# Kernel tuning notes

Measured on AMD Instinct MI355X. Metric: run time of the kernel, lower is better.

Reference implementation:

```python
import jax, jax.numpy as jnp
import numpy as np
from jax import lax

STEPLIM = 10
TOL = 1e-4
EPS = 1e-12


def setup_inputs() -> dict:
    key = jax.random.key(0)
    k1, k2 = jax.random.split(key)
    psrc = jax.random.normal(k1, (8, 2048, 3), dtype=jnp.float32)
    ptgt = jax.random.normal(k2, (8, 2048, 3), dtype=jnp.float32)
    return {"psrc": psrc, "ptgt": ptgt}


def _kabsch(p, q):
    # Rigid transform (R, t) minimizing ||q - (R p + t)|| via SVD (Kabsch).
    # p, q: [B, N, 3] matched point pairs.
    cs = jnp.mean(p, axis=-2, keepdims=True)  # [B,1,3]
    ct = jnp.mean(q, axis=-2, keepdims=True)
    H = jnp.einsum('bni,bnj->bij', p - cs, q - ct)  # [B,3,3]
    U, S, Vt = jnp.linalg.svd(H, full_matrices=False)
    V = jnp.swapaxes(Vt, -1, -2)
    Ut = jnp.swapaxes(U, -1, -2)
    d = jnp.sign(jnp.linalg.det(V @ Ut))  # [B], reflection fix
    scale = jnp.stack([jnp.ones_like(d), jnp.ones_like(d), d], axis=-1)  # [B,3]
    R = (V * scale[:, None, :]) @ Ut  # V @ diag(1,1,d) @ U^T
    t = ct[:, 0, :] - jnp.einsum('bij,bj->bi', R, cs[:, 0, :])
    return R, t


def _nn(pc, ptgt):
    # Brute-force 1-NN of each pc point in ptgt. Returns (dist [B,Ns], idx [B,Ns]).
    # GEMM-form squared distances: ||a||^2 + ||b||^2 - 2 a.b
    a2 = jnp.sum(pc * pc, axis=-1)  # [B,Ns]
    b2 = jnp.sum(ptgt * ptgt, axis=-1)  # [B,Nt]
    d2 = a2[:, :, None] + b2[:, None, :] - 2.0 * jnp.einsum('bnd,bmd->bnm', pc, ptgt)
    d2 = jnp.maximum(d2, EPS)
    idx = jnp.argmin(d2, axis=-1)  # [B,Ns]
    dist = jnp.sqrt(jnp.min(d2, axis=-1))
    return dist, idx


def reference(psrc, ptgt):
    B = psrc.shape[0]

    def step(carry, _):
        pc, err, done = carry
        dist, idx = _nn(pc, ptgt)
        errnew = jnp.mean(dist, axis=-1)  # [B]
        done_new = jnp.logical_or(done, jnp.all(jnp.abs(errnew - err) < TOL))
        matched = jnp.take_along_axis(ptgt, idx[:, :, None], axis=1)  # [B,Ns,3]
        R, t = _kabsch(pc, matched)
        pc_upd = jnp.einsum('bij,bnj->bni', R, pc) + t[:, None, :]
        pc_new = jnp.where(done_new, pc, pc_upd)
        err_new = jnp.where(done_new, err, errnew)
        return (pc_new, err_new, done_new), None

    init = (psrc, jnp.zeros((B,), psrc.dtype), jnp.array(False))
    (pc_final, _, _), _ = lax.scan(step, init, None, length=STEPLIM)

    # Final transform from original psrc to converged point cloud.
    R, t = _kabsch(psrc, pc_final)
    return jnp.concatenate([R, t[:, :, None]], axis=-1)  # [B,3,4]
```

## Files before the change

### kernel.cpp

```cpp
#include <hip/hip_runtime.h>
#include <math.h>

#define NB 8
#define NP 2048
#define GRID 256
#define THREADS 512
#define TOLF 1e-4f
#define EPSF 1e-12f

#define AL(p)   __hip_atomic_load((p), __ATOMIC_RELAXED, __HIP_MEMORY_SCOPE_AGENT)
#define AS(p,v) __hip_atomic_store((p), (v), __ATOMIC_RELAXED, __HIP_MEMORY_SCOPE_AGENT)

__device__ inline float3 xform_pt(const float* __restrict__ T,
                                  float x, float y, float z) {
    float3 r;
    r.x = fmaf(T[0], x, fmaf(T[1], y, fmaf(T[2], z, T[9])));
    r.y = fmaf(T[3], x, fmaf(T[4], y, fmaf(T[5], z, T[10])));
    r.z = fmaf(T[6], x, fmaf(T[7], y, fmaf(T[8], z, T[11])));
    return r;
}

__device__ void kabsch3x3(const double Spq[9], const double Sp[3], const double Sq[3],
                          double R[9], double t[3]) {
    const double invN = 1.0 / (double)NP;
    double cs[3], ct[3];
#pragma unroll
    for (int i = 0; i < 3; ++i) { cs[i] = Sp[i] * invN; ct[i] = Sq[i] * invN; }
    double Hd[9];
#pragma unroll
    for (int i = 0; i < 3; ++i)
#pragma unroll
        for (int j = 0; j < 3; ++j)
            Hd[i * 3 + j] = Spq[i * 3 + j] - (double)NP * cs[i] * ct[j];

    float Bc[3][3], V[3][3];
#pragma unroll
    for (int j = 0; j < 3; ++j)
#pragma unroll
        for (int i = 0; i < 3; ++i) {
            Bc[j][i] = (float)Hd[i * 3 + j];
            V[j][i]  = (i == j) ? 1.0f : 0.0f;
        }
    for (int sweep = 0; sweep < 12; ++sweep) {
        bool rotated = false;
        for (int p = 0; p < 2; ++p)
            for (int q = p + 1; q < 3; ++q) {
                float app = 0.f, aqq = 0.f, apq = 0.f;
#pragma unroll
                for (int i = 0; i < 3; ++i) {
                    app = fmaf(Bc[p][i], Bc[p][i], app);
                    aqq = fmaf(Bc[q][i], Bc[q][i], aqq);
                    apq = fmaf(Bc[p][i], Bc[q][i], apq);
                }
                if (apq * apq > 1e-24f + 1e-12f * app * aqq) {
                    rotated = true;
                    float tau = (aqq - app) / (2.0f * apq);
                    float tt  = (tau >= 0.f ? 1.0f : -1.0f) /
                                (fabsf(tau) + sqrtf(fmaf(tau, tau, 1.0f)));
                    float c   = 1.0f / sqrtf(fmaf(tt, tt, 1.0f));
                    float sn  = c * tt;
#pragma unroll
                    for (int i = 0; i < 3; ++i) {
                        float bp = Bc[p][i], bq = Bc[q][i];
                        Bc[p][i] = c * bp - sn * bq;
                        Bc[q][i] = sn * bp + c * bq;
                        float vp = V[p][i], vq = V[q][i];
                        V[p][i] = c * vp - sn * vq;
                        V[q][i] = sn * vp + c * vq;
                    }
                }
            }
        if (!rotated) break;
    }
    float sv[3], U[3][3];
#pragma unroll
    for (int j = 0; j < 3; ++j) {
        sv[j] = sqrtf(Bc[j][0] * Bc[j][0] + Bc[j][1] * Bc[j][1] + Bc[j][2] * Bc[j][2]);
        float inv = sv[j] > 0.f ? 1.0f / sv[j] : 0.f;
#pragma unroll
        for (int i = 0; i < 3; ++i) U[j][i] = Bc[j][i] * inv;
    }
    double detH = Hd[0] * (Hd[4] * Hd[8] - Hd[5] * Hd[7])
                - Hd[1] * (Hd[3] * Hd[8] - Hd[5] * Hd[6])
                + Hd[2] * (Hd[3] * Hd[7] - Hd[4] * Hd[6]);
    float d = (detH >= 0.0) ? 1.0f : -1.0f;
    int o[3] = {0, 1, 2};
    if (sv[o[0]] < sv[o[1]]) { int tmp = o[0]; o[0] = o[1]; o[1] = tmp; }
    if (sv[o[0]] < sv[o[2]]) { int tmp = o[0]; o[0] = o[2]; o[2] = tmp; }
    if (sv[o[1]] < sv[o[2]]) { int tmp = o[1]; o[1] = o[2]; o[2] = tmp; }
    float sg[3] = {1.0f, 1.0f, d};
#pragma unroll
    for (int i = 0; i < 3; ++i)
#pragma unroll
        for (int j = 0; j < 3; ++j) {
            float acc = 0.0f;
#pragma unroll
            for (int k = 0; k < 3; ++k) acc += sg[k] * V[o[k]][i] * U[o[k]][j];
            R[i * 3 + j] = (double)acc;
        }
#pragma unroll
    for (int i = 0; i < 3; ++i)
        t[i] = ct[i] - (R[i * 3 + 0] * cs[0] + R[i * 3 + 1] * cs[1] + R[i * 3 + 2] * cs[2]);
}

__global__ __launch_bounds__(256) void icp_init(unsigned* __restrict__ flags) {
    flags[threadIdx.x] = 0u;
}

__global__ __launch_bounds__(THREADS, 1) void icp_main(
        const float* __restrict__ psrc, const float* __restrict__ ptgt,
        double* __restrict__ partial,
        unsigned* __restrict__ flags,
        double* __restrict__ Tcs,
        unsigned* __restrict__ cbits) {
    __shared__ float4 tg[2112];
    __shared__ float4 ps[64];
    __shared__ float2 comb[64][66];
    __shared__ float  TcL[12];
    __shared__ double TcA[12];

    const int tid   = threadIdx.x;
    const int blk   = blockIdx.x;
    const int b     = blk >> 5;
    const int sc    = blk & 31;
    const int slice = tid & 63;
    const int g     = tid >> 6;

    float errL = 0.0f;

    const float* tb = ptgt + b * NP * 3;
    for (int j = tid; j < NP; j += THREADS) {
        float tx = tb[3 * j + 0], ty = tb[3 * j + 1], tz = tb[3 * j + 2];
        tg[j + (j >> 5)] = make_float4(tx, ty, tz,
                                       0.5f * (tx * tx + ty * ty + tz * tz));
    }
    if (tid < 12) {
        float idv = (tid == 0 || tid == 4 || tid == 8) ? 1.0f : 0.0f;
        TcL[tid] = idv;
        TcA[tid] = (double)idv;
        if (sc == 0) AS(&Tcs[(b * 11 + 0) * 12 + tid], (double)idv);
    }
    __syncthreads();

    for (int it = 1; it <= 10; ++it) {
        if (tid < 64) {
            const float* pp = psrc + (b * NP + sc * 64 + tid) * 3;
            float3 P = xform_pt(TcL, pp[0], pp[1], pp[2]);
            ps[tid] = make_float4(P.x, P.y, P.z,
                                  P.x * P.x + P.y * P.y + P.z * P.z);
        }
        __syncthreads();

        float sx[8], sy[8], sz[8], sm[8];
        int jm[8];
#pragma unroll
        for (int k = 0; k < 8; ++k) {
            float4 P = ps[g * 8 + k];
            sx[k] = P.x; sy[k] = P.y; sz[k] = P.z;
            sm[k] = INFINITY; jm[k] = 0;
        }
        const int base = slice * 33, jbase = slice * 32;
#pragma unroll 4
        for (int i = 0; i < 32; ++i) {
            float4 t = tg[base + i];
            int j = jbase + i;
#pragma unroll
            for (int k = 0; k < 8; ++k) {
                float s = fmaf(-sx[k], t.x, fmaf(-sy[k], t.y, fmaf(-sz[k], t.z, t.w)));
                if (s < sm[k]) { sm[k] = s; jm[k] = j; }
            }
        }
#pragma unroll
        for (int k = 0; k < 8; ++k)
            comb[slice][g * 8 + k] = make_float2(sm[k], __int_as_float(jm[k]));
        __syncthreads();

        double* pbase = partial + (size_t)(it & 1) * GRID * 16;

        if (tid < 64) {
            float fb = INFINITY; int fj = 0;
#pragma unroll 8
            for (int q = 0; q < 64; ++q) {
                float2 e = comb[q][tid];
                if (e.x < fb) { fb = e.x; fj = __float_as_int(e.y); }
            }
            float4 P = ps[tid];
            float d2 = fmaf(2.0f, fb, P.w);
            float dist = sqrtf(fmaxf(d2, EPSF));
            float4 Q = tg[fj + (fj >> 5)];

            double v[16];
            v[0] = dist;
            v[1] = P.x; v[2] = P.y; v[3] = P.z;
            v[4] = Q.x; v[5] = Q.y; v[6] = Q.z;
            v[7]  = (double)P.x * Q.x; v[8]  = (double)P.x * Q.y; v[9]  = (double)P.x * Q.z;
            v[10] = (double)P.y * Q.x; v[11] = (double)P.y * Q.y; v[12] = (double)P.y * Q.z;
            v[13] = (double)P.z * Q.x; v[14] = (double)P.z * Q.y; v[15] = (double)P.z * Q.z;
#pragma unroll
            for (int k = 0; k < 16; ++k) {
                double x = v[k];
#pragma unroll
                for (int off = 32; off > 0; off >>= 1) x += __shfl_down(x, off);
                v[k] = x;
            }
            if (tid == 0) {
                double* dst = pbase + blk * 16;
#pragma unroll
                for (int k = 0; k < 16; ++k) AS(dst + k, v[k]);
                asm volatile("s_waitcnt vmcnt(0)" ::: "memory");
                AS(&flags[blk], (unsigned)it);
            }
        } else if (tid < 128) {
            int l = tid - 64;
            bool ok;
            do {
                ok = (l < 32) ? (AL(&flags[b * 32 + l]) >= (unsigned)it) : true;
                if (!__all(ok)) __builtin_amdgcn_s_sleep(1); else break;
            } while (true);
        }
        __syncthreads();

        if (tid < 32) {
            double acc[16];
            const double* pp2 = pbase + (b * 32 + tid) * 16;
#pragma unroll
            for (int k = 0; k < 16; ++k) acc[k] = AL(pp2 + k);
#pragma unroll
            for (int k = 0; k < 16; ++k) {
                double x = acc[k];
                x += __shfl_down(x, 16);
                x += __shfl_down(x, 8);
                x += __shfl_down(x, 4);
                x += __shfl_down(x, 2);
                x += __shfl_down(x, 1);
                acc[k] = x;
            }
            if (tid == 0) {
                float errnew = (float)(acc[0] * (1.0 / (double)NP));
                unsigned cb = (fabsf(errnew - errL) < TOLF) ? 1u : 0u;
                errL = errnew;
                double R[9], t[3];
                kabsch3x3(&acc[7], &acc[1], &acc[4], R, t);
                double To[12];
#pragma unroll
                for (int k = 0; k < 12; ++k) To[k] = TcA[k];
#pragma unroll
                for (int i = 0; i < 3; ++i) {
#pragma unroll
                    for (int j = 0; j < 3; ++j)
                        TcA[i * 3 + j] = R[i * 3 + 0] * To[0 + j]
                                       + R[i * 3 + 1] * To[3 + j]
                                       + R[i * 3 + 2] * To[6 + j];
                    TcA[9 + i] = R[i * 3 + 0] * To[9] + R[i * 3 + 1] * To[10]
                               + R[i * 3 + 2] * To[11] + t[i];
                }
                if (sc == 0) {
#pragma unroll
                    for (int k = 0; k < 12; ++k)
                        AS(&Tcs[(b * 11 + it) * 12 + k], TcA[k]);
                    AS(&cbits[b * 16 + it], cb);
                }
            }
        }
        __syncthreads();
        if (tid < 12) TcL[tid] = (float)TcA[tid];
        __syncthreads();
    }
}

__global__ __launch_bounds__(64) void icp_resolve(const double* __restrict__ Tcs,
                                                  const unsigned* __restrict__ cbits,
                                                  float* __restrict__ out) {
    __shared__ int ksel;
    int tid = threadIdx.x;
    if (tid == 0) {
        int sel = 10;
        for (int t = 1; t <= 10; ++t) {
            bool all = true;
            for (int b2 = 0; b2 < NB; ++b2) all = all && (cbits[b2 * 16 + t] != 0u);
            if (all) { sel = t - 1; break; }
        }
        ksel = sel;
    }
    __syncthreads();
    if (tid < NB) {
        const double* T = Tcs + ((size_t)tid * 11 + ksel) * 12;
        float* o = out + tid * 12;
#pragma unroll
        for (int i = 0; i < 3; ++i) {
#pragma unroll
            for (int j = 0; j < 3; ++j) o[i * 4 + j] = (float)T[i * 3 + j];
            o[i * 4 + 3] = (float)T[9 + i];
        }
    }
}

extern "C" void kernel_launch(void* const* d_in, const int* in_sizes, int n_in,
                              void* d_out, int out_size, void* d_ws, size_t ws_size,
                              hipStream_t stream) {
    const float* psrc = (const float*)d_in[0];
    const float* ptgt = (const float*)d_in[1];
    float* out = (float*)d_out;

    char* ws = (char*)d_ws;
    size_t off = 0;
    double* partial = (double*)(ws + off); off += 2ull * GRID * 16 * sizeof(double);
    unsigned* flags = (unsigned*)(ws + off); off += GRID * sizeof(unsigned);
    double* Tcs   = (double*)(ws + off);   off += (size_t)NB * 11 * 12 * sizeof(double);
    unsigned* cbits = (unsigned*)(ws + off); off += NB * 16 * sizeof(unsigned);

    icp_init<<<1, 256, 0, stream>>>(flags);
    icp_main<<<GRID, THREADS, 0, stream>>>(psrc, ptgt, partial, flags, Tcs, cbits);
    icp_resolve<<<1, 64, 0, stream>>>(Tcs, cbits, out);
}
```

Before: 183.0 us.

## Use packed FP32 FMA with SoA target layout and two-stage argmin reduction

Target points are stored in shared memory as separate x/y/z/w arrays of float pairs, so the nearest-neighbour inner loop can score two targets per instruction with v_pk_fma_f32. The cross-slice argmin is split into two stages: all threads first reduce 8 entries each into a smaller buffer, then 64 threads reduce 8 entries instead of 64. This cuts VALU work in the distance loop and serial latency in the reduction, at the cost of an extra barrier and slightly different tie-breaking.

```diff
diff --git a/kernel.cpp b/kernel.cpp
--- a/kernel.cpp
+++ b/kernel.cpp
@@ -10,6 +10,8 @@
 
 #define AL(p)   __hip_atomic_load((p), __ATOMIC_RELAXED, __HIP_MEMORY_SCOPE_AGENT)
 #define AS(p,v) __hip_atomic_store((p), (v), __ATOMIC_RELAXED, __HIP_MEMORY_SCOPE_AGENT)
+
+typedef __attribute__((ext_vector_type(2))) float f32x2;
 
 __device__ inline float3 xform_pt(const float* __restrict__ T,
                                   float x, float y, float z) {
@@ -113,9 +115,10 @@
         unsigned* __restrict__ flags,
         double* __restrict__ Tcs,
         unsigned* __restrict__ cbits) {
-    __shared__ float4 tg[2112];
+    __shared__ f32x2 tgx[1088], tgy[1088], tgz[1088], tgw[1088];
     __shared__ float4 ps[64];
     __shared__ float2 comb[64][66];
+    __shared__ float2 comb2[8][66];
     __shared__ float  TcL[12];
     __shared__ double TcA[12];
 
@@ -131,8 +134,11 @@
     const float* tb = ptgt + b * NP * 3;
     for (int j = tid; j < NP; j += THREADS) {
         float tx = tb[3 * j + 0], ty = tb[3 * j + 1], tz = tb[3 * j + 2];
-        tg[j + (j >> 5)] = make_float4(tx, ty, tz,
-                                       0.5f * (tx * tx + ty * ty + tz * tz));
+        int fi = (j >> 5) * 34 + (j & 31);
+        ((float*)tgx)[fi] = tx;
+        ((float*)tgy)[fi] = ty;
+        ((float*)tgz)[fi] = tz;
+        ((float*)tgw)[fi] = 0.5f * (tx * tx + ty * ty + tz * tz);
     }
     if (tid < 12) {
         float idv = (tid == 0 || tid == 4 || tid == 8) ? 1.0f : 0.0f;
@@ -151,23 +157,38 @@
         }
         __syncthreads();
 
-        float sx[8], sy[8], sz[8], sm[8];
+        f32x2 nx[8], ny[8], nz[8];
+        float sm[8];
         int jm[8];
 #pragma unroll
         for (int k = 0; k < 8; ++k) {
             float4 P = ps[g * 8 + k];
-            sx[k] = P.x; sy[k] = P.y; sz[k] = P.z;
+            nx[k] = (f32x2){-P.x, -P.x};
+            ny[k] = (f32x2){-P.y, -P.y};
+            nz[k] = (f32x2){-P.z, -P.z};
             sm[k] = INFINITY; jm[k] = 0;
         }
-        const int base = slice * 33, jbase = slice * 32;
+        const int pb = slice * 17, jbase = slice * 32;
 #pragma unroll 4
-        for (int i = 0; i < 32; ++i) {
-            float4 t = tg[base + i];
-            int j = jbase + i;
+        for (int p = 0; p < 16; ++p) {
+            f32x2 tx2 = tgx[pb + p];
+            f32x2 ty2 = tgy[pb + p];
+            f32x2 tz2 = tgz[pb + p];
+            f32x2 tw2 = tgw[pb + p];
+            int jj = jbase + 2 * p;
 #pragma unroll
             for (int k = 0; k < 8; ++k) {
-                float s = fmaf(-sx[k], t.x, fmaf(-sy[k], t.y, fmaf(-sz[k], t.z, t.w)));
-                if (s < sm[k]) { sm[k] = s; jm[k] = j; }
+                f32x2 a;
+                asm("v_pk_fma_f32 %0, %1, %2, %3"
+                    : "=v"(a) : "v"(nz[k]), "v"(tz2), "v"(tw2));
+                asm("v_pk_fma_f32 %0, %1, %2, %0"
+                    : "+v"(a) : "v"(ny[k]), "v"(ty2));
+                asm("v_pk_fma_f32 %0, %1, %2, %0"
+                    : "+v"(a) : "v"(nx[k]), "v"(tx2));
+                float m2 = fminf(a.x, a.y);
+                int js = (a.x <= a.y) ? jj : jj + 1;
+                if (m2 < sm[k]) jm[k] = js;
+                sm[k] = fminf(sm[k], m2);
             }
         }
 #pragma unroll
@@ -175,27 +196,43 @@
             comb[slice][g * 8 + k] = make_float2(sm[k], __int_as_float(jm[k]));
         __syncthreads();
 
+        {
+            int l = tid & 63;
+            float fb = INFINITY; int fj = 0;
+#pragma unroll
+            for (int q = 0; q < 8; ++q) {
+                float2 e = comb[g * 8 + q][l];
+                if (e.x < fb) { fb = e.x; fj = __float_as_int(e.y); }
+            }
+            comb2[g][l] = make_float2(fb, __int_as_float(fj));
+        }
+        __syncthreads();
+
         double* pbase = partial + (size_t)(it & 1) * GRID * 16;
 
         if (tid < 64) {
             float fb = INFINITY; int fj = 0;
-#pragma unroll 8
-            for (int q = 0; q < 64; ++q) {
-                float2 e = comb[q][tid];
+#pragma unroll
+            for (int q = 0; q < 8; ++q) {
+                float2 e = comb2[q][tid];
                 if (e.x < fb) { fb = e.x; fj = __float_as_int(e.y); }
             }
             float4 P = ps[tid];
             float d2 = fmaf(2.0f, fb, P.w);
             float dist = sqrtf(fmaxf(d2, EPSF));
-            float4 Q = tg[fj + (fj >> 5)];
+            int qp = (fj >> 5) * 17 + ((fj & 31) >> 1);
+            f32x2 qx2 = tgx[qp], qy2 = tgy[qp], qz2 = tgz[qp];
+            float Qx = (fj & 1) ? qx2.y : qx2.x;
+            float Qy = (fj & 1) ? qy2.y : qy2.x;
+            float Qz = (fj & 1) ? qz2.y : qz2.x;
 
             double v[16];
             v[0] = dist;
             v[1] = P.x; v[2] = P.y; v[3] = P.z;
-            v[4] = Q.x; v[5] = Q.y; v[6] = Q.z;
-            v[7]  = (double)P.x * Q.x; v[8]  = (double)P.x * Q.y; v[9]  = (double)P.x * Q.z;
-            v[10] = (double)P.y * Q.x; v[11] = (double)P.y * Q.y; v[12] = (double)P.y * Q.z;
-            v[13] = (double)P.z * Q.x; v[14] = (double)P.z * Q.y; v[15] = (double)P.z * Q.z;
+            v[4] = Qx;  v[5] = Qy;  v[6] = Qz;
+            v[7]  = (double)P.x * Qx; v[8]  = (double)P.x * Qy; v[9]  = (double)P.x * Qz;
+            v[10] = (double)P.y * Qx; v[11] = (double)P.y * Qy; v[12] = (double)P.y * Qz;
+            v[13] = (double)P.z * Qx; v[14] = (double)P.z * Qy; v[15] = (double)P.z * Qz;
 #pragma unroll
             for (int k = 0; k < 16; ++k) {
                 double x = v[k];
```

Measured after the change: 180.3 us. About the same (-1.4%).

## Make every wavefront reduce partials and compute Kabsch redundantly, removing block barriers

Applied to the files above, without the earlier changes.

Each wavefront now polls the cross-block flags itself, reduces the 32 partials and runs the 3x3 Kabsch update. The result is broadcast through wavefront shuffles and the transform is kept in registers, so the trailing __syncthreads barriers and shared transform arrays go away. Source points are transformed directly from global memory, removing the shared ps staging. The 64-way argmin combine is split into two 8-way stages with an extra barrier. Block-to-batch mapping becomes interleaved (b = blk & 7), trading redundant double-precision work and more global polling for fewer barriers and a shorter serial tail.

```diff
diff --git a/kernel.cpp b/kernel.cpp
--- a/kernel.cpp
+++ b/kernel.cpp
@@ -114,19 +114,27 @@
         double* __restrict__ Tcs,
         unsigned* __restrict__ cbits) {
     __shared__ float4 tg[2112];
-    __shared__ float4 ps[64];
     __shared__ float2 comb[64][66];
-    __shared__ float  TcL[12];
-    __shared__ double TcA[12];
+    __shared__ float2 comb2[8][66];
 
     const int tid   = threadIdx.x;
     const int blk   = blockIdx.x;
-    const int b     = blk >> 5;
-    const int sc    = blk & 31;
+    const int b     = blk & 7;
+    const int sc    = blk >> 3;
+    const int lid   = b * 32 + sc;
     const int slice = tid & 63;
-    const int g     = tid >> 6;
-
-    float errL = 0.0f;
+    const int w     = tid >> 6;
+    const int lane  = tid & 63;
+
+    float  TcL[12];
+    double TcA[12];
+    float  errL = 0.0f;
+#pragma unroll
+    for (int k = 0; k < 12; ++k) {
+        float idv = (k == 0 || k == 4 || k == 8) ? 1.0f : 0.0f;
+        TcL[k] = idv;
+        TcA[k] = (double)idv;
+    }
 
     const float* tb = ptgt + b * NP * 3;
     for (int j = tid; j < NP; j += THREADS) {
@@ -134,28 +142,21 @@
         tg[j + (j >> 5)] = make_float4(tx, ty, tz,
                                        0.5f * (tx * tx + ty * ty + tz * tz));
     }
-    if (tid < 12) {
+    if (sc == 0 && tid < 12) {
         float idv = (tid == 0 || tid == 4 || tid == 8) ? 1.0f : 0.0f;
-        TcL[tid] = idv;
-        TcA[tid] = (double)idv;
-        if (sc == 0) AS(&Tcs[(b * 11 + 0) * 12 + tid], (double)idv);
+        AS(&Tcs[(b * 11 + 0) * 12 + tid], (double)idv);
     }
     __syncthreads();
 
+    const float* sp = psrc + (b * NP + sc * 64) * 3;
+
     for (int it = 1; it <= 10; ++it) {
-        if (tid < 64) {
-            const float* pp = psrc + (b * NP + sc * 64 + tid) * 3;
-            float3 P = xform_pt(TcL, pp[0], pp[1], pp[2]);
-            ps[tid] = make_float4(P.x, P.y, P.z,
-                                  P.x * P.x + P.y * P.y + P.z * P.z);
-        }
-        __syncthreads();
-
         float sx[8], sy[8], sz[8], sm[8];
         int jm[8];
 #pragma unroll
         for (int k = 0; k < 8; ++k) {
-            float4 P = ps[g * 8 + k];
+            const float* pp = sp + (w * 8 + k) * 3;
+            float3 P = xform_pt(TcL, pp[0], pp[1], pp[2]);
             sx[k] = P.x; sy[k] = P.y; sz[k] = P.z;
             sm[k] = INFINITY; jm[k] = 0;
         }
@@ -172,20 +173,33 @@
         }
 #pragma unroll
         for (int k = 0; k < 8; ++k)
-            comb[slice][g * 8 + k] = make_float2(sm[k], __int_as_float(jm[k]));
+            comb[slice][w * 8 + k] = make_float2(sm[k], __int_as_float(jm[k]));
         __syncthreads();
 
+        {
+            float fb = INFINITY; int fj = 0;
+#pragma unroll
+            for (int q = 0; q < 8; ++q) {
+                float2 e = comb[w * 8 + q][lane];
+                if (e.x < fb) { fb = e.x; fj = __float_as_int(e.y); }
+            }
+            comb2[w][lane] = make_float2(fb, __int_as_float(fj));
+        }
+        __syncthreads();
+
         double* pbase = partial + (size_t)(it & 1) * GRID * 16;
 
-        if (tid < 64) {
+        if (w == 0) {
             float fb = INFINITY; int fj = 0;
-#pragma unroll 8
-            for (int q = 0; q < 64; ++q) {
-                float2 e = comb[q][tid];
+#pragma unroll
+            for (int q = 0; q < 8; ++q) {
+                float2 e = comb2[q][lane];
                 if (e.x < fb) { fb = e.x; fj = __float_as_int(e.y); }
             }
-            float4 P = ps[tid];
-            float d2 = fmaf(2.0f, fb, P.w);
+            const float* pp = sp + lane * 3;
+            float3 P = xform_pt(TcL, pp[0], pp[1], pp[2]);
+            float Pw = P.x * P.x + P.y * P.y + P.z * P.z;
+            float d2 = fmaf(2.0f, fb, Pw);
             float dist = sqrtf(fmaxf(d2, EPSF));
             float4 Q = tg[fj + (fj >> 5)];
 
@@ -203,68 +217,72 @@
                 for (int off = 32; off > 0; off >>= 1) x += __shfl_down(x, off);
                 v[k] = x;
             }
-            if (tid == 0) {
-                double* dst = pbase + blk * 16;
+            if (lane == 0) {
+                double* dst = pbase + lid * 16;
 #pragma unroll
                 for (int k = 0; k < 16; ++k) AS(dst + k, v[k]);
                 asm volatile("s_waitcnt vmcnt(0)" ::: "memory");
-                AS(&flags[blk], (unsigned)it);
-            }
-        } else if (tid < 128) {
-            int l = tid - 64;
+                AS(&flags[lid], (unsigned)it);
+            }
+        }
+
+        {
             bool ok;
             do {
-                ok = (l < 32) ? (AL(&flags[b * 32 + l]) >= (unsigned)it) : true;
+                ok = (lane < 32) ? (AL(&flags[b * 32 + lane]) >= (unsigned)it) : true;
                 if (!__all(ok)) __builtin_amdgcn_s_sleep(1); else break;
             } while (true);
         }
-        __syncthreads();
-
-        if (tid < 32) {
+        {
             double acc[16];
-            const double* pp2 = pbase + (b * 32 + tid) * 16;
-#pragma unroll
-            for (int k = 0; k < 16; ++k) acc[k] = AL(pp2 + k);
-#pragma unroll
-            for (int k = 0; k < 16; ++k) {
-                double x = acc[k];
-                x += __shfl_down(x, 16);
-                x += __shfl_down(x, 8);
-                x += __shfl_down(x, 4);
-                x += __shfl_down(x, 2);
-                x += __shfl_down(x, 1);
-                acc[k] = x;
-            }
-            if (tid == 0) {
-                float errnew = (float)(acc[0] * (1.0 / (double)NP));
-                unsigned cb = (fabsf(errnew - errL) < TOLF) ? 1u : 0u;
-                errL = errnew;
-                double R[9], t[3];
-                kabsch3x3(&acc[7], &acc[1], &acc[4], R, t);
-                double To[12];
-#pragma unroll
-                for (int k = 0; k < 12; ++k) To[k] = TcA[k];
-#pragma unroll
-                for (int i = 0; i < 3; ++i) {
-#pragma unroll
-                    for (int j = 0; j < 3; ++j)
-                        TcA[i * 3 + j] = R[i * 3 + 0] * To[0 + j]
-                                       + R[i * 3 + 1] * To[3 + j]
-                                       + R[i * 3 + 2] * To[6 + j];
-                    TcA[9 + i] = R[i * 3 + 0] * To[9] + R[i * 3 + 1] * To[10]
-                               + R[i * 3 + 2] * To[11] + t[i];
+            if (lane < 32) {
+                const double* pp2 = pbase + (b * 32 + lane) * 16;
+#pragma unroll
+                for (int k = 0; k < 16; ++k) acc[k] = AL(pp2 + k);
+#pragma unroll
+                for (int k = 0; k < 16; ++k) {
+                    double x = acc[k];
+                    x += __shfl_down(x, 16);
+                    x += __shfl_down(x, 8);
+                    x += __shfl_down(x, 4);
+                    x += __shfl_down(x, 2);
+                    x += __shfl_down(x, 1);
+                    acc[k] = x;
                 }
-                if (sc == 0) {
-#pragma unroll
-                    for (int k = 0; k < 12; ++k)
-                        AS(&Tcs[(b * 11 + it) * 12 + k], TcA[k]);
-                    AS(&cbits[b * 16 + it], cb);
+                if (lane == 0) {
+                    float errnew = (float)(acc[0] * (1.0 / (double)NP));
+                    unsigned cb = (fabsf(errnew - errL) < TOLF) ? 1u : 0u;
+                    errL = errnew;
+                    double R[9], t[3];
+                    kabsch3x3(&acc[7], &acc[1], &acc[4], R, t);
+                    double To[12];
+#pragma unroll
+                    for (int k = 0; k < 12; ++k) To[k] = TcA[k];
+#pragma unroll
+                    for (int i = 0; i < 3; ++i) {
+#pragma unroll
+                        for (int j = 0; j < 3; ++j)
+                            TcA[i * 3 + j] = R[i * 3 + 0] * To[0 + j]
+                                           + R[i * 3 + 1] * To[3 + j]
+                                           + R[i * 3 + 2] * To[6 + j];
+                        TcA[9 + i] = R[i * 3 + 0] * To[9] + R[i * 3 + 1] * To[10]
+                                   + R[i * 3 + 2] * To[11] + t[i];
+                    }
+                    if (sc == 0 && w == 0) {
+#pragma unroll
+                        for (int k = 0; k < 12; ++k)
+                            AS(&Tcs[(b * 11 + it) * 12 + k], TcA[k]);
+                        AS(&cbits[b * 16 + it], cb);
+                    }
                 }
             }
-        }
-        __syncthreads();
-        if (tid < 12) TcL[tid] = (float)TcA[tid];
-        __syncthreads();
+#pragma unroll
+            for (int k = 0; k < 12; ++k) {
+                double nv = __shfl(TcA[k], 0);
+                TcA[k] = nv;
+                TcL[k] = (float)nv;
+            }
+        }
     }
 }
 
```

New measurement: 232.9 us. +27.3%, slower.
